# Optimization experiments

Hardware: AMD Instinct MI355X
Metric: run time of the kernel (lower is better)

Reference implementation:

```python
import jax, jax.numpy as jnp
import numpy as np

# dims: R ranks, B batch, HQ q-heads, HKV kv-heads-per-rank, G = HQ//HKV group size,
# D head dim, S kv splits (hardcoded 32 in module), L max kv len per rank, P pages per rank
R, B, HQ, HKV, D, S, L, P = 4, 16, 32, 2, 128, 32, 2048, 32768
G = HQ // HKV  # kv_group_num = num_q_heads // num_kv_heads_per_rank
NEG = -jnp.inf


def setup_inputs() -> dict:
    key = jax.random.key(0)
    k1, k2, k3, k4, k5 = jax.random.split(key, 5)
    q = jax.random.normal(k1, (B, HQ, D), jnp.float32)
    k_cache = jax.random.normal(k2, (R, P, HKV, D), jnp.float32)
    v_cache = jax.random.normal(k3, (R, P, HKV, D), jnp.float32)
    block_table = jax.random.randint(k4, (R, B, L), 0, P, jnp.int32)
    # per-rank kv lengths; min 64 to keep all math well-defined
    kv_lens_per_rank = jax.random.randint(k5, (R, B), 64, L + 1, jnp.int32)
    return dict(q=q, k_cache=k_cache, v_cache=v_cache,
                block_table=block_table, kv_lens_per_rank=kv_lens_per_rank)


def _attend(q, k_cache, v_cache, block_table, kv_lens):
    scale = D ** -0.5
    # page_size == 1: block_table entries are token slots in the per-rank cache.
    ridx = jnp.arange(R)[:, None, None]
    k = k_cache[ridx, block_table]  # [R,B,L,HKV,D]
    v = v_cache[ridx, block_table]  # [R,B,L,HKV,D]

    # GQA: q head h uses local kv head h // G on each rank
    qg = q.reshape(B, HKV, G, D)
    scores = jnp.einsum('bkgd,rblkd->rbkgl', qg, k) * scale  # [R,B,HKV,G,L]

    n = jnp.arange(L)
    valid = n[None, None, :] < kv_lens[..., None]            # [R,B,L]
    scores = jnp.where(valid[:, :, None, None, :], scores, NEG)

    # stage 1: split-KV. split s covers [s*per, (s+1)*per) with per = ceil(len/S)
    per = -(-kv_lens // S)                                   # [R,B]
    sid = n[None, None, :] // per[..., None]                 # [R,B,L]

    lse_s = []
    for s in range(S):  # fixed small loop over NUM_KV_SPLITS
        m = jnp.where((sid == s)[:, :, None, None, :], scores, NEG)
        lse_s.append(jax.scipy.special.logsumexp(m, axis=-1))  # [R,B,HKV,G]
    lse_s = jnp.stack(lse_s)  # [S,R,B,HKV,G]; empty splits -> -inf (kernel skips them)

    # stage 2: local combine over splits. NOTE (faithful to kernel): local_out stores
    # the UNNORMALIZED accumulator sum_s exp(lse_s - m_r) * o_s together with
    # lse_r = m_r + log(sum_s exp(lse_s - m_r)), where m_r = max_s lse_s.
    m_r = jnp.max(lse_s, axis=0)                              # [R,B,HKV,G]
    lse_r = m_r + jnp.log(jnp.sum(jnp.exp(lse_s - m_r), axis=0))
    # sum_s exp(lse_s - m_r) * (softmax_s @ v_s) == sum_n exp(score_n - m_r) * v_n
    p = jnp.exp(scores - m_r[..., None])                      # masked entries -> 0
    acc_r = jnp.einsum('rbkgl,rblkd->rbkgd', p, v)            # [R,B,HKV,G,D]

    acc = acc_r.reshape(R, B, HQ, D)
    lse = lse_r.reshape(R, B, HQ)

    # stage 3: global lse-weighted combine across ranks (online softmax == this)
    M = jnp.max(lse, axis=0)                                  # [B,HQ]
    w = jnp.exp(lse - M)                                      # [R,B,HQ]
    out = jnp.sum(w[..., None] * acc, axis=0) / jnp.sum(w, axis=0)[..., None]
    return out  # [B,HQ,D]


def reference(q, k_cache, v_cache, block_table, kv_lens_per_rank):
    return _attend(q, k_cache, v_cache, block_table, kv_lens_per_rank)
```

## Files before the change

### kernel.cpp

```cpp
#include <hip/hip_runtime.h>
#include <math.h>

#define R_ 4
#define B_ 16
#define HQ_ 32
#define HKV_ 2
#define G_ 16
#define D_ 128
#define S_ 32
#define L_ 2048
#define P_ 32768
#define C_ 8
#define NSPL_ 4
#define TS_ 64
#define NEGINF (-INFINITY)

#define WS_LSE   0
#define WS_CM    65536
#define WS_CACC  (65536 + 16384)

__global__ __launch_bounds__(256) void fd_stage1(
    const float* __restrict__ q, const float* __restrict__ kc,
    const float* __restrict__ vc, const int* __restrict__ bt,
    const int* __restrict__ lens,
    float* __restrict__ lse_split, float* __restrict__ chunk_m,
    float* __restrict__ chunk_acc)
{
  const int t   = threadIdx.x;
  const int blk = blockIdx.x;
  const int c   = blk & 7;
  const int hkv = (blk >> 3) & 1;
  const int b   = (blk >> 4) & 15;
  const int r   = blk >> 8;

  const int len = lens[r*B_ + b];
  const int per = (len + S_ - 1) >> 5;

  __shared__ float q_s[G_][D_+4];
  __shared__ float k_s[TS_][D_+4];
  __shared__ float p_s[G_][TS_];
  __shared__ float alpha_s[G_];
  __shared__ int   page_s[TS_];

  {
    const float* qb = q + (b*HQ_ + hkv*G_)*D_;
    int f4 = t;
    #pragma unroll
    for (int i = 0; i < 2; ++i, f4 += 256) {
      int g = f4 >> 5, dd = (f4 & 31) * 4;
      *(float4*)&q_s[g][dd] = *(const float4*)&qb[g*D_ + dd];
    }
  }

  const int sg = t >> 4;
  const int nl = t & 15;
  const int d4 = (t & 31) * 4;
  const int gp = t >> 5;

  float  m_run = NEGINF;
  float4 acc0 = make_float4(0.f,0.f,0.f,0.f);
  float4 acc1 = make_float4(0.f,0.f,0.f,0.f);

  const int* btb   = bt + (r*B_ + b)*L_;
  const int kvbase = r*(P_*HKV_*D_) + hkv*D_;
  float* lse_out = lse_split + ((r*B_ + b)*HKV_ + hkv)*(S_*G_);

  for (int j = 0; j < NSPL_; ++j) {
    const int s  = c*NSPL_ + j;
    const int n0 = s*per;
    const int tn = min(per, len - n0);
    if (tn <= 0) {
      if (t < G_) lse_out[s*G_ + t] = NEGINF;
      continue;
    }
    __syncthreads();
    if (t < tn) page_s[t] = btb[n0 + t];
    __syncthreads();
    for (int row = t >> 5; row < tn; row += 8) {
      const float4 kx = *(const float4*)&kc[kvbase + page_s[row]*(HKV_*D_) + ((t & 31)*4)];
      *(float4*)&k_s[row][(t & 31)*4] = kx;
    }
    __syncthreads();

    float s0 = 0.f, s1 = 0.f, s2 = 0.f, s3 = 0.f;
    #pragma unroll 8
    for (int d = 0; d < D_; d += 4) {
      const float4 q4 = *(const float4*)&q_s[sg][d];
      const float4 k0 = *(const float4*)&k_s[nl     ][d];
      const float4 k1 = *(const float4*)&k_s[nl + 16][d];
      const float4 k2 = *(const float4*)&k_s[nl + 32][d];
      const float4 k3 = *(const float4*)&k_s[nl + 48][d];
      s0 += q4.x*k0.x + q4.y*k0.y + q4.z*k0.z + q4.w*k0.w;
      s1 += q4.x*k1.x + q4.y*k1.y + q4.z*k1.z + q4.w*k1.w;
      s2 += q4.x*k2.x + q4.y*k2.y + q4.z*k2.z + q4.w*k2.w;
      s3 += q4.x*k3.x + q4.y*k3.y + q4.z*k3.z + q4.w*k3.w;
    }
    const float sc = 0.08838834764831845f;
    float sv0 = (nl      < tn) ? s0*sc : NEGINF;
    float sv1 = (nl + 16 < tn) ? s1*sc : NEGINF;
    float sv2 = (nl + 32 < tn) ? s2*sc : NEGINF;
    float sv3 = (nl + 48 < tn) ? s3*sc : NEGINF;

    float pm = fmaxf(fmaxf(sv0, sv1), fmaxf(sv2, sv3));
    #pragma unroll
    for (int off = 1; off < 16; off <<= 1)
      pm = fmaxf(pm, __shfl_xor(pm, off));
    float ps = __expf(sv0 - pm) + __expf(sv1 - pm) + __expf(sv2 - pm) + __expf(sv3 - pm);
    #pragma unroll
    for (int off = 1; off < 16; off <<= 1)
      ps += __shfl_xor(ps, off);
    const float lse  = pm + __logf(ps);
    const float newm = fmaxf(m_run, pm);
    if (nl == 0) {
      lse_out[s*G_ + sg] = lse;
      alpha_s[sg] = __expf(m_run - newm);
    }
    m_run = newm;
    p_s[sg][nl]      = __expf(sv0 - newm);
    p_s[sg][nl + 16] = __expf(sv1 - newm);
    p_s[sg][nl + 32] = __expf(sv2 - newm);
    p_s[sg][nl + 48] = __expf(sv3 - newm);
    __syncthreads();

    const float a0 = alpha_s[gp], a1 = alpha_s[gp + 8];
    acc0.x *= a0; acc0.y *= a0; acc0.z *= a0; acc0.w *= a0;
    acc1.x *= a1; acc1.y *= a1; acc1.z *= a1; acc1.w *= a1;
    #pragma unroll 4
    for (int n = 0; n < tn; ++n) {
      const float4 v4 = *(const float4*)&vc[kvbase + page_s[n]*(HKV_*D_) + d4];
      const float p0 = p_s[gp][n], p1 = p_s[gp + 8][n];
      acc0.x += p0*v4.x; acc0.y += p0*v4.y; acc0.z += p0*v4.z; acc0.w += p0*v4.w;
      acc1.x += p1*v4.x; acc1.y += p1*v4.y; acc1.z += p1*v4.z; acc1.w += p1*v4.w;
    }
  }

  if (nl == 0)
    chunk_m[(((r*B_ + b)*HKV_ + hkv)*C_ + c)*G_ + sg] = m_run;
  float* ca = chunk_acc + (size_t)((((r*B_ + b)*HKV_ + hkv)*C_ + c)*G_) * D_;
  *(float4*)&ca[gp*D_ + d4]       = acc0;
  *(float4*)&ca[(gp + 8)*D_ + d4] = acc1;
}

__global__ __launch_bounds__(128) void fd_stage2(
    const float* __restrict__ lse_split, const float* __restrict__ chunk_m,
    const float* __restrict__ chunk_acc, float* __restrict__ out)
{
  const int bh  = blockIdx.x;
  const int b   = bh >> 5, h = bh & 31;
  const int hkv = h >> 4, g = h & 15;
  const int d   = threadIdx.x;

  float m_r[R_], lse_r[R_];
  #pragma unroll
  for (int r = 0; r < R_; ++r) {
    const float* ls = lse_split + ((r*B_ + b)*HKV_ + hkv)*(S_*G_) + g;
    float m = NEGINF;
    #pragma unroll
    for (int s2 = 0; s2 < S_; ++s2) m = fmaxf(m, ls[s2*G_]);
    float sum = 0.f;
    #pragma unroll
    for (int s2 = 0; s2 < S_; ++s2) sum += __expf(ls[s2*G_] - m);
    m_r[r]   = m;
    lse_r[r] = m + __logf(sum);
  }
  const float M = fmaxf(fmaxf(lse_r[0], lse_r[1]), fmaxf(lse_r[2], lse_r[3]));
  float denom = 0.f, o = 0.f;
  #pragma unroll
  for (int r = 0; r < R_; ++r) {
    const float w = __expf(lse_r[r] - M);
    denom += w;
    const float* cm = chunk_m  + ((r*B_ + b)*HKV_ + hkv)*(C_*G_) + g;
    const float* ca = chunk_acc + (size_t)(((r*B_ + b)*HKV_ + hkv)*(C_*G_) + g) * D_ + d;
    float a = 0.f;
    #pragma unroll
    for (int cc2 = 0; cc2 < C_; ++cc2)
      a += __expf(cm[cc2*G_] - m_r[r]) * ca[(size_t)cc2 * (G_*D_)];
    o += w * a;
  }
  out[(size_t)bh*D_ + d] = o / denom;
}

extern "C" void kernel_launch(void* const* d_in, const int* in_sizes, int n_in,
                              void* d_out, int out_size, void* d_ws, size_t ws_size,
                              hipStream_t stream) {
  const float* q   = (const float*)d_in[0];
  const float* kc  = (const float*)d_in[1];
  const float* vc  = (const float*)d_in[2];
  const int*   bt  = (const int*)d_in[3];
  const int*   len = (const int*)d_in[4];
  float* out = (float*)d_out;
  float* ws  = (float*)d_ws;

  float* lse_split = ws + WS_LSE;
  float* chunk_m   = ws + WS_CM;
  float* chunk_acc = ws + WS_CACC;

  fd_stage1<<<dim3(R_*B_*HKV_*C_), dim3(256), 0, stream>>>(
      q, kc, vc, bt, len, lse_split, chunk_m, chunk_acc);
  fd_stage2<<<dim3(B_*HQ_), dim3(128), 0, stream>>>(
      lse_split, chunk_m, chunk_acc, out);
}
```

Baseline: 342.8 us.

## Launch one stage-1 block per KV split and skip empty key sub-tiles

Stage 1 becomes a template on splits-per-block. When the workspace is large enough it launches one block per split (1024 blocks instead of 256), so more blocks run at once and the running-max rescaling is dropped. The score loop also skips the 16-row key groups that lie beyond the split length. In exchange, stage 2 has to combine 32 chunk accumulators instead of 8 with a loop that is no longer unrolled, which adds workspace traffic.

Result: slower. 356.1 us (+3.9%).

```diff
diff --git a/kernel.cpp b/kernel.cpp
--- a/kernel.cpp
+++ b/kernel.cpp
@@ -10,15 +10,11 @@
 #define S_ 32
 #define L_ 2048
 #define P_ 32768
-#define C_ 8
-#define NSPL_ 4
 #define TS_ 64
 #define NEGINF (-INFINITY)
 
-#define WS_LSE   0
-#define WS_CM    65536
-#define WS_CACC  (65536 + 16384)
-
+
+template<int NSPL>
 __global__ __launch_bounds__(256) void fd_stage1(
     const float* __restrict__ q, const float* __restrict__ kc,
     const float* __restrict__ vc, const int* __restrict__ bt,
@@ -26,12 +22,14 @@
     float* __restrict__ lse_split, float* __restrict__ chunk_m,
     float* __restrict__ chunk_acc)
 {
-  const int t   = threadIdx.x;
-  const int blk = blockIdx.x;
-  const int c   = blk & 7;
-  const int hkv = (blk >> 3) & 1;
-  const int b   = (blk >> 4) & 15;
-  const int r   = blk >> 8;
+  constexpr int CH = S_ / NSPL;
+  const int t    = threadIdx.x;
+  const int blk  = blockIdx.x;
+  const int c    = blk % CH;
+  const int rest = blk / CH;
+  const int hkv  = rest & 1;
+  const int b    = (rest >> 1) & 15;
+  const int r    = rest >> 5;
 
   const int len = lens[r*B_ + b];
   const int per = (len + S_ - 1) >> 5;
@@ -65,8 +63,8 @@
   const int kvbase = r*(P_*HKV_*D_) + hkv*D_;
   float* lse_out = lse_split + ((r*B_ + b)*HKV_ + hkv)*(S_*G_);
 
-  for (int j = 0; j < NSPL_; ++j) {
-    const int s  = c*NSPL_ + j;
+  for (int j = 0; j < NSPL; ++j) {
+    const int s  = c*NSPL + j;
     const int n0 = s*per;
     const int tn = min(per, len - n0);
     if (tn <= 0) {
@@ -82,18 +80,25 @@
     }
     __syncthreads();
 
+    const int KN = (tn + 15) >> 4;
     float s0 = 0.f, s1 = 0.f, s2 = 0.f, s3 = 0.f;
-    #pragma unroll 8
+    #pragma unroll 4
     for (int d = 0; d < D_; d += 4) {
       const float4 q4 = *(const float4*)&q_s[sg][d];
-      const float4 k0 = *(const float4*)&k_s[nl     ][d];
-      const float4 k1 = *(const float4*)&k_s[nl + 16][d];
-      const float4 k2 = *(const float4*)&k_s[nl + 32][d];
-      const float4 k3 = *(const float4*)&k_s[nl + 48][d];
+      const float4 k0 = *(const float4*)&k_s[nl][d];
       s0 += q4.x*k0.x + q4.y*k0.y + q4.z*k0.z + q4.w*k0.w;
-      s1 += q4.x*k1.x + q4.y*k1.y + q4.z*k1.z + q4.w*k1.w;
-      s2 += q4.x*k2.x + q4.y*k2.y + q4.z*k2.z + q4.w*k2.w;
-      s3 += q4.x*k3.x + q4.y*k3.y + q4.z*k3.z + q4.w*k3.w;
+      if (KN > 1) {
+        const float4 k1 = *(const float4*)&k_s[nl + 16][d];
+        s1 += q4.x*k1.x + q4.y*k1.y + q4.z*k1.z + q4.w*k1.w;
+      }
+      if (KN > 2) {
+        const float4 k2 = *(const float4*)&k_s[nl + 32][d];
+        s2 += q4.x*k2.x + q4.y*k2.y + q4.z*k2.z + q4.w*k2.w;
+      }
+      if (KN > 3) {
+        const float4 k3 = *(const float4*)&k_s[nl + 48][d];
+        s3 += q4.x*k3.x + q4.y*k3.y + q4.z*k3.z + q4.w*k3.w;
+      }
     }
     const float sc = 0.08838834764831845f;
     float sv0 = (nl      < tn) ? s0*sc : NEGINF;
@@ -110,21 +115,23 @@
     for (int off = 1; off < 16; off <<= 1)
       ps += __shfl_xor(ps, off);
     const float lse  = pm + __logf(ps);
-    const float newm = fmaxf(m_run, pm);
+    const float newm = (NSPL > 1) ? fmaxf(m_run, pm) : pm;
     if (nl == 0) {
       lse_out[s*G_ + sg] = lse;
-      alpha_s[sg] = __expf(m_run - newm);
+      if (NSPL > 1) alpha_s[sg] = __expf(m_run - newm);
     }
     m_run = newm;
-    p_s[sg][nl]      = __expf(sv0 - newm);
-    p_s[sg][nl + 16] = __expf(sv1 - newm);
-    p_s[sg][nl + 32] = __expf(sv2 - newm);
-    p_s[sg][nl + 48] = __expf(sv3 - newm);
-    __syncthreads();
-
-    const float a0 = alpha_s[gp], a1 = alpha_s[gp + 8];
-    acc0.x *= a0; acc0.y *= a0; acc0.z *= a0; acc0.w *= a0;
-    acc1.x *= a1; acc1.y *= a1; acc1.z *= a1; acc1.w *= a1;
+    p_s[sg][nl] = __expf(sv0 - newm);
+    if (KN > 1) p_s[sg][nl + 16] = __expf(sv1 - newm);
+    if (KN > 2) p_s[sg][nl + 32] = __expf(sv2 - newm);
+    if (KN > 3) p_s[sg][nl + 48] = __expf(sv3 - newm);
+    __syncthreads();
+
+    if (NSPL > 1) {
+      const float a0 = alpha_s[gp], a1 = alpha_s[gp + 8];
+      acc0.x *= a0; acc0.y *= a0; acc0.z *= a0; acc0.w *= a0;
+      acc1.x *= a1; acc1.y *= a1; acc1.z *= a1; acc1.w *= a1;
+    }
     #pragma unroll 4
     for (int n = 0; n < tn; ++n) {
       const float4 v4 = *(const float4*)&vc[kvbase + page_s[n]*(HKV_*D_) + d4];
@@ -135,15 +142,15 @@
   }
 
   if (nl == 0)
-    chunk_m[(((r*B_ + b)*HKV_ + hkv)*C_ + c)*G_ + sg] = m_run;
-  float* ca = chunk_acc + (size_t)((((r*B_ + b)*HKV_ + hkv)*C_ + c)*G_) * D_;
+    chunk_m[(((r*B_ + b)*HKV_ + hkv)*CH + c)*G_ + sg] = m_run;
+  float* ca = chunk_acc + (size_t)((((r*B_ + b)*HKV_ + hkv)*CH + c)*G_) * D_;
   *(float4*)&ca[gp*D_ + d4]       = acc0;
   *(float4*)&ca[(gp + 8)*D_ + d4] = acc1;
 }
 
 __global__ __launch_bounds__(128) void fd_stage2(
     const float* __restrict__ lse_split, const float* __restrict__ chunk_m,
-    const float* __restrict__ chunk_acc, float* __restrict__ out)
+    const float* __restrict__ chunk_acc, float* __restrict__ out, int CH)
 {
   const int bh  = blockIdx.x;
   const int b   = bh >> 5, h = bh & 31;
@@ -169,11 +176,10 @@
   for (int r = 0; r < R_; ++r) {
     const float w = __expf(lse_r[r] - M);
     denom += w;
-    const float* cm = chunk_m  + ((r*B_ + b)*HKV_ + hkv)*(C_*G_) + g;
-    const float* ca = chunk_acc + (size_t)(((r*B_ + b)*HKV_ + hkv)*(C_*G_) + g) * D_ + d;
+    const float* cm = chunk_m  + (((r*B_ + b)*HKV_ + hkv)*CH)*G_ + g;
+    const float* ca = chunk_acc + (size_t)((((r*B_ + b)*HKV_ + hkv)*CH)*G_ + g) * D_ + d;
     float a = 0.f;
-    #pragma unroll
-    for (int cc2 = 0; cc2 < C_; ++cc2)
+    for (int cc2 = 0; cc2 < CH; ++cc2)
       a += __expf(cm[cc2*G_] - m_r[r]) * ca[(size_t)cc2 * (G_*D_)];
     o += w * a;
   }
@@ -191,12 +197,26 @@
   float* out = (float*)d_out;
   float* ws  = (float*)d_ws;
 
-  float* lse_split = ws + WS_LSE;
-  float* chunk_m   = ws + WS_CM;
-  float* chunk_acc = ws + WS_CACC;
-
-  fd_stage1<<<dim3(R_*B_*HKV_*C_), dim3(256), 0, stream>>>(
-      q, kc, vc, bt, len, lse_split, chunk_m, chunk_acc);
-  fd_stage2<<<dim3(B_*HQ_), dim3(128), 0, stream>>>(
-      lse_split, chunk_m, chunk_acc, out);
+  const size_t lse_f = (size_t)R_*B_*HKV_*S_*G_;
+  const size_t need32 = (lse_f + (size_t)R_*B_*HKV_*32*G_ +
+                         (size_t)R_*B_*HKV_*32*G_*D_) * 4;
+  if (ws_size >= need32) {
+    const int CH = 32;
+    float* lse_split = ws;
+    float* chunk_m   = ws + lse_f;
+    float* chunk_acc = chunk_m + (size_t)R_*B_*HKV_*CH*G_;
+    fd_stage1<1><<<dim3(R_*B_*HKV_*CH), dim3(256), 0, stream>>>(
+        q, kc, vc, bt, len, lse_split, chunk_m, chunk_acc);
+    fd_stage2<<<dim3(B_*HQ_), dim3(128), 0, stream>>>(
+        lse_split, chunk_m, chunk_acc, out, CH);
+  } else {
+    const int CH = 8;
+    float* lse_split = ws;
+    float* chunk_m   = ws + lse_f;
+    float* chunk_acc = chunk_m + (size_t)R_*B_*HKV_*CH*G_;
+    fd_stage1<4><<<dim3(R_*B_*HKV_*CH), dim3(256), 0, stream>>>(
+        q, kc, vc, bt, len, lse_split, chunk_m, chunk_acc);
+    fd_stage2<<<dim3(B_*HQ_), dim3(128), 0, stream>>>(
+        lse_split, chunk_m, chunk_acc, out, CH);
+  }
 }
```

## Give each KV split its own block and use fp16 for QK dots and partials

Applied to the files above, without the earlier changes.

Stage 1 now launches one block per (rank, batch, kv-head, split) instead of one per group of four splits. This raises the block count fourfold and removes the online rescaling across splits inside a block. Q and K are converted to fp16 in shared memory and multiplied with packed fdot2. Per-split partial accumulators are stored in fp16 and combined over all 32 splits in stage 2. This adds parallelism and cuts shared-memory and workspace traffic, at the cost of fp16 precision loss in the scores and partial outputs and a larger stage-2 reduction.

Measured after the change: 307.7 us. 10.3% less time.

```diff
diff --git a/kernel.cpp b/kernel.cpp
--- a/kernel.cpp
+++ b/kernel.cpp
@@ -10,140 +10,160 @@
 #define S_ 32
 #define L_ 2048
 #define P_ 32768
-#define C_ 8
-#define NSPL_ 4
 #define TS_ 64
+#define KSTR 136
+#define PSTR 18
 #define NEGINF (-INFINITY)
 
-#define WS_LSE   0
-#define WS_CM    65536
-#define WS_CACC  (65536 + 16384)
-
-__global__ __launch_bounds__(256) void fd_stage1(
+typedef _Float16 h2 __attribute__((ext_vector_type(2)));
+typedef _Float16 h4 __attribute__((ext_vector_type(4)));
+typedef _Float16 h8 __attribute__((ext_vector_type(8)));
+
+#if defined(__has_builtin)
+#  if __has_builtin(__builtin_amdgcn_fdot2)
+#    define FDOT2(a,b,c) __builtin_amdgcn_fdot2((a),(b),(c),false)
+#  endif
+#endif
+#ifndef FDOT2
+static __device__ __forceinline__ float fdot2_sw(h2 a, h2 b, float c) {
+  return c + (float)a.x*(float)b.x + (float)a.y*(float)b.y;
+}
+#  define FDOT2(a,b,c) fdot2_sw((a),(b),(c))
+#endif
+
+
+__global__ __launch_bounds__(256, 6) void fd_stage1(
     const float* __restrict__ q, const float* __restrict__ kc,
     const float* __restrict__ vc, const int* __restrict__ bt,
     const int* __restrict__ lens,
     float* __restrict__ lse_split, float* __restrict__ chunk_m,
-    float* __restrict__ chunk_acc)
+    _Float16* __restrict__ chunk_acc)
 {
   const int t   = threadIdx.x;
   const int blk = blockIdx.x;
-  const int c   = blk & 7;
-  const int hkv = (blk >> 3) & 1;
-  const int b   = (blk >> 4) & 15;
-  const int r   = blk >> 8;
+  const int s   = blk & 31;
+  const int hkv = (blk >> 5) & 1;
+  const int b   = (blk >> 6) & 15;
+  const int r   = blk >> 10;
 
   const int len = lens[r*B_ + b];
-  const int per = (len + S_ - 1) >> 5;
-
-  __shared__ float q_s[G_][D_+4];
-  __shared__ float k_s[TS_][D_+4];
-  __shared__ float p_s[G_][TS_];
-  __shared__ float alpha_s[G_];
-  __shared__ int   page_s[TS_];
+  const int per = (len + 31) >> 5;
+  const int n0  = s*per;
+  const int tn  = min(per, len - n0);
+
+  float* lse_out = lse_split + ((r*B_ + b)*HKV_ + hkv)*(S_*G_);
+  const int cmbase = (((r*B_ + b)*HKV_ + hkv)*S_ + s)*G_;
+  _Float16* ca = chunk_acc + (size_t)(((r*B_ + b)*HKV_ + hkv)*S_ + s)*(G_*D_);
+
+  if (tn <= 0) {
+    if (t < G_) { lse_out[s*G_ + t] = NEGINF; chunk_m[cmbase + t] = NEGINF; }
+    h8 z = {(_Float16)0,(_Float16)0,(_Float16)0,(_Float16)0,
+            (_Float16)0,(_Float16)0,(_Float16)0,(_Float16)0};
+    *(h8*)&ca[t*8] = z;
+    return;
+  }
+
+  __shared__ _Float16 q_s[G_][KSTR];
+  __shared__ _Float16 k_s[TS_][KSTR];
+  __shared__ float    p_s[TS_][PSTR];
 
   {
     const float* qb = q + (b*HQ_ + hkv*G_)*D_;
     int f4 = t;
     #pragma unroll
     for (int i = 0; i < 2; ++i, f4 += 256) {
-      int g = f4 >> 5, dd = (f4 & 31) * 4;
-      *(float4*)&q_s[g][dd] = *(const float4*)&qb[g*D_ + dd];
-    }
-  }
-
-  const int sg = t >> 4;
-  const int nl = t & 15;
-  const int d4 = (t & 31) * 4;
-  const int gp = t >> 5;
-
-  float  m_run = NEGINF;
-  float4 acc0 = make_float4(0.f,0.f,0.f,0.f);
-  float4 acc1 = make_float4(0.f,0.f,0.f,0.f);
+      const int g = f4 >> 5, dd = (f4 & 31)*4;
+      const float4 v = *(const float4*)&qb[g*D_ + dd];
+      h4 hv; hv.x=(_Float16)v.x; hv.y=(_Float16)v.y; hv.z=(_Float16)v.z; hv.w=(_Float16)v.w;
+      *(h4*)&q_s[g][dd] = hv;
+    }
+  }
 
   const int* btb   = bt + (r*B_ + b)*L_;
   const int kvbase = r*(P_*HKV_*D_) + hkv*D_;
-  float* lse_out = lse_split + ((r*B_ + b)*HKV_ + hkv)*(S_*G_);
-
-  for (int j = 0; j < NSPL_; ++j) {
-    const int s  = c*NSPL_ + j;
-    const int n0 = s*per;
-    const int tn = min(per, len - n0);
-    if (tn <= 0) {
-      if (t < G_) lse_out[s*G_ + t] = NEGINF;
-      continue;
-    }
-    __syncthreads();
-    if (t < tn) page_s[t] = btb[n0 + t];
-    __syncthreads();
-    for (int row = t >> 5; row < tn; row += 8) {
-      const float4 kx = *(const float4*)&kc[kvbase + page_s[row]*(HKV_*D_) + ((t & 31)*4)];
-      *(float4*)&k_s[row][(t & 31)*4] = kx;
-    }
-    __syncthreads();
-
-    float s0 = 0.f, s1 = 0.f, s2 = 0.f, s3 = 0.f;
-    #pragma unroll 8
-    for (int d = 0; d < D_; d += 4) {
-      const float4 q4 = *(const float4*)&q_s[sg][d];
-      const float4 k0 = *(const float4*)&k_s[nl     ][d];
-      const float4 k1 = *(const float4*)&k_s[nl + 16][d];
-      const float4 k2 = *(const float4*)&k_s[nl + 32][d];
-      const float4 k3 = *(const float4*)&k_s[nl + 48][d];
-      s0 += q4.x*k0.x + q4.y*k0.y + q4.z*k0.z + q4.w*k0.w;
-      s1 += q4.x*k1.x + q4.y*k1.y + q4.z*k1.z + q4.w*k1.w;
-      s2 += q4.x*k2.x + q4.y*k2.y + q4.z*k2.z + q4.w*k2.w;
-      s3 += q4.x*k3.x + q4.y*k3.y + q4.z*k3.z + q4.w*k3.w;
-    }
-    const float sc = 0.08838834764831845f;
-    float sv0 = (nl      < tn) ? s0*sc : NEGINF;
-    float sv1 = (nl + 16 < tn) ? s1*sc : NEGINF;
-    float sv2 = (nl + 32 < tn) ? s2*sc : NEGINF;
-    float sv3 = (nl + 48 < tn) ? s3*sc : NEGINF;
-
-    float pm = fmaxf(fmaxf(sv0, sv1), fmaxf(sv2, sv3));
+
+  {
+    const int lane = t & 31, rw = t >> 5;
+    for (int row = rw; row < tn; row += 8) {
+      const int pg = btb[n0 + row];
+      const float4 v = *(const float4*)&kc[kvbase + pg*(HKV_*D_) + lane*4];
+      h4 hv; hv.x=(_Float16)v.x; hv.y=(_Float16)v.y; hv.z=(_Float16)v.z; hv.w=(_Float16)v.w;
+      *(h4*)&k_s[row][lane*4] = hv;
+    }
+  }
+  __syncthreads();
+
+  const int sg = t >> 4, nl = t & 15;
+  const int KN = (tn + 15) >> 4;
+  float s0 = 0.f, s1 = 0.f, s2 = 0.f, s3 = 0.f;
+  #pragma unroll 4
+  for (int d8 = 0; d8 < 16; ++d8) {
+    const h8 q8 = *(const h8*)&q_s[sg][d8*8];
+    const h8 k0 = *(const h8*)&k_s[nl][d8*8];
     #pragma unroll
-    for (int off = 1; off < 16; off <<= 1)
-      pm = fmaxf(pm, __shfl_xor(pm, off));
-    float ps = __expf(sv0 - pm) + __expf(sv1 - pm) + __expf(sv2 - pm) + __expf(sv3 - pm);
-    #pragma unroll
-    for (int off = 1; off < 16; off <<= 1)
-      ps += __shfl_xor(ps, off);
-    const float lse  = pm + __logf(ps);
-    const float newm = fmaxf(m_run, pm);
-    if (nl == 0) {
-      lse_out[s*G_ + sg] = lse;
-      alpha_s[sg] = __expf(m_run - newm);
-    }
-    m_run = newm;
-    p_s[sg][nl]      = __expf(sv0 - newm);
-    p_s[sg][nl + 16] = __expf(sv1 - newm);
-    p_s[sg][nl + 32] = __expf(sv2 - newm);
-    p_s[sg][nl + 48] = __expf(sv3 - newm);
-    __syncthreads();
-
-    const float a0 = alpha_s[gp], a1 = alpha_s[gp + 8];
-    acc0.x *= a0; acc0.y *= a0; acc0.z *= a0; acc0.w *= a0;
-    acc1.x *= a1; acc1.y *= a1; acc1.z *= a1; acc1.w *= a1;
-    #pragma unroll 4
-    for (int n = 0; n < tn; ++n) {
-      const float4 v4 = *(const float4*)&vc[kvbase + page_s[n]*(HKV_*D_) + d4];
-      const float p0 = p_s[gp][n], p1 = p_s[gp + 8][n];
-      acc0.x += p0*v4.x; acc0.y += p0*v4.y; acc0.z += p0*v4.z; acc0.w += p0*v4.w;
-      acc1.x += p1*v4.x; acc1.y += p1*v4.y; acc1.z += p1*v4.z; acc1.w += p1*v4.w;
-    }
-  }
-
-  if (nl == 0)
-    chunk_m[(((r*B_ + b)*HKV_ + hkv)*C_ + c)*G_ + sg] = m_run;
-  float* ca = chunk_acc + (size_t)((((r*B_ + b)*HKV_ + hkv)*C_ + c)*G_) * D_;
-  *(float4*)&ca[gp*D_ + d4]       = acc0;
-  *(float4*)&ca[(gp + 8)*D_ + d4] = acc1;
+    for (int j = 0; j < 4; ++j) s0 = FDOT2(((const h2*)&q8)[j], ((const h2*)&k0)[j], s0);
+    if (KN > 1) {
+      const h8 k1 = *(const h8*)&k_s[nl + 16][d8*8];
+      #pragma unroll
+      for (int j = 0; j < 4; ++j) s1 = FDOT2(((const h2*)&q8)[j], ((const h2*)&k1)[j], s1);
+    }
+    if (KN > 2) {
+      const h8 k2 = *(const h8*)&k_s[nl + 32][d8*8];
+      #pragma unroll
+      for (int j = 0; j < 4; ++j) s2 = FDOT2(((const h2*)&q8)[j], ((const h2*)&k2)[j], s2);
+    }
+    if (KN > 3) {
+      const h8 k3 = *(const h8*)&k_s[nl + 48][d8*8];
+      #pragma unroll
+      for (int j = 0; j < 4; ++j) s3 = FDOT2(((const h2*)&q8)[j], ((const h2*)&k3)[j], s3);
+    }
+  }
+  const float sc = 0.08838834764831845f;
+  const float sv0 = (nl      < tn) ? s0*sc : NEGINF;
+  const float sv1 = (nl + 16 < tn) ? s1*sc : NEGINF;
+  const float sv2 = (nl + 32 < tn) ? s2*sc : NEGINF;
+  const float sv3 = (nl + 48 < tn) ? s3*sc : NEGINF;
+
+  float pm = fmaxf(fmaxf(sv0, sv1), fmaxf(sv2, sv3));
+  #pragma unroll
+  for (int off = 1; off < 16; off <<= 1) pm = fmaxf(pm, __shfl_xor(pm, off));
+  float ps = __expf(sv0 - pm) + __expf(sv1 - pm) + __expf(sv2 - pm) + __expf(sv3 - pm);
+  #pragma unroll
+  for (int off = 1; off < 16; off <<= 1) ps += __shfl_xor(ps, off);
+
+  if (nl == 0) {
+    lse_out[s*G_ + sg] = pm + __logf(ps);
+    chunk_m[cmbase + sg] = pm;
+  }
+
+  p_s[nl][sg] = __expf(sv0 - pm);
+  if (KN > 1) p_s[nl + 16][sg] = __expf(sv1 - pm);
+  if (KN > 2) p_s[nl + 32][sg] = __expf(sv2 - pm);
+  if (KN > 3) p_s[nl + 48][sg] = __expf(sv3 - pm);
+  __syncthreads();
+
+  const int d4 = (t & 31)*4;
+  const int g2 = (t >> 5)*2;
+  float4 a0 = make_float4(0.f,0.f,0.f,0.f);
+  float4 a1 = make_float4(0.f,0.f,0.f,0.f);
+  #pragma unroll 4
+  for (int n = 0; n < tn; ++n) {
+    const int pg = btb[n0 + n];
+    const float4 v4 = *(const float4*)&vc[kvbase + pg*(HKV_*D_) + d4];
+    const float2 pp = *(const float2*)&p_s[n][g2];
+    a0.x += pp.x*v4.x; a0.y += pp.x*v4.y; a0.z += pp.x*v4.z; a0.w += pp.x*v4.w;
+    a1.x += pp.y*v4.x; a1.y += pp.y*v4.y; a1.z += pp.y*v4.z; a1.w += pp.y*v4.w;
+  }
+
+  h4 o0; o0.x=(_Float16)a0.x; o0.y=(_Float16)a0.y; o0.z=(_Float16)a0.z; o0.w=(_Float16)a0.w;
+  h4 o1; o1.x=(_Float16)a1.x; o1.y=(_Float16)a1.y; o1.z=(_Float16)a1.z; o1.w=(_Float16)a1.w;
+  *(h4*)&ca[g2*D_ + d4]       = o0;
+  *(h4*)&ca[(g2 + 1)*D_ + d4] = o1;
 }
 
 __global__ __launch_bounds__(128) void fd_stage2(
     const float* __restrict__ lse_split, const float* __restrict__ chunk_m,
-    const float* __restrict__ chunk_acc, float* __restrict__ out)
+    const _Float16* __restrict__ chunk_acc, float* __restrict__ out)
 {
   const int bh  = blockIdx.x;
   const int b   = bh >> 5, h = bh & 31;
@@ -155,10 +175,10 @@
   for (int r = 0; r < R_; ++r) {
     const float* ls = lse_split + ((r*B_ + b)*HKV_ + hkv)*(S_*G_) + g;
     float m = NEGINF;
-    #pragma unroll
+    #pragma unroll 8
     for (int s2 = 0; s2 < S_; ++s2) m = fmaxf(m, ls[s2*G_]);
     float sum = 0.f;
-    #pragma unroll
+    #pragma unroll 8
     for (int s2 = 0; s2 < S_; ++s2) sum += __expf(ls[s2*G_] - m);
     m_r[r]   = m;
     lse_r[r] = m + __logf(sum);
@@ -169,12 +189,13 @@
   for (int r = 0; r < R_; ++r) {
     const float w = __expf(lse_r[r] - M);
     denom += w;
-    const float* cm = chunk_m  + ((r*B_ + b)*HKV_ + hkv)*(C_*G_) + g;
-    const float* ca = chunk_acc + (size_t)(((r*B_ + b)*HKV_ + hkv)*(C_*G_) + g) * D_ + d;
+    const float* cm = chunk_m + (((r*B_ + b)*HKV_ + hkv)*S_)*G_ + g;
+    const _Float16* ca = chunk_acc
+        + (size_t)(((r*B_ + b)*HKV_ + hkv)*S_)*(G_*D_) + g*D_ + d;
     float a = 0.f;
-    #pragma unroll
-    for (int cc2 = 0; cc2 < C_; ++cc2)
-      a += __expf(cm[cc2*G_] - m_r[r]) * ca[(size_t)cc2 * (G_*D_)];
+    #pragma unroll 8
+    for (int c = 0; c < S_; ++c)
+      a += __expf(cm[c*G_] - m_r[r]) * (float)ca[(size_t)c*(G_*D_)];
     o += w * a;
   }
   out[(size_t)bh*D_ + d] = o / denom;
@@ -191,11 +212,12 @@
   float* out = (float*)d_out;
   float* ws  = (float*)d_ws;
 
-  float* lse_split = ws + WS_LSE;
-  float* chunk_m   = ws + WS_CM;
-  float* chunk_acc = ws + WS_CACC;
-
-  fd_stage1<<<dim3(R_*B_*HKV_*C_), dim3(256), 0, stream>>>(
+  const size_t lse_f = (size_t)R_*B_*HKV_*S_*G_;
+  float*    lse_split = ws;
+  float*    chunk_m   = ws + lse_f;
+  _Float16* chunk_acc = (_Float16*)(ws + 2*lse_f);
+
+  fd_stage1<<<dim3(R_*B_*HKV_*S_), dim3(256), 0, stream>>>(
       q, kc, vc, bt, len, lse_split, chunk_m, chunk_acc);
   fd_stage2<<<dim3(B_*HQ_), dim3(128), 0, stream>>>(
       lse_split, chunk_m, chunk_acc, out);
```
